# Optimization experiments

Hardware: AMD Instinct MI355X
Metric: run time of the kernel (lower is better)

Reference implementation:

```python
import jax, jax.numpy as jnp
import numpy as np

H = 256   # hidden_size
IN = 2    # adding-problem input features
B, T = 128, 1024


def setup_inputs() -> dict:
    key = jax.random.key(0)
    ks = jax.random.split(key, 12)
    sc = 1.0 / np.sqrt(H)
    u = lambda k, shape: jax.random.uniform(k, shape, minval=-sc, maxval=sc, dtype=jnp.float32)
    return {
        "x": jax.random.normal(ks[0], (B, T, IN), dtype=jnp.float32),
        # GRU weights (torch layout: [3H, in], gate order r, z, n)
        "W_ih": u(ks[1], (3 * H, IN)),
        "W_hh": u(ks[2], (3 * H, H)),
        "b_ih": u(ks[3], (3 * H,)),
        "b_hh": u(ks[4], (3 * H,)),
        # adaptive momentum coefficient beta_t = sigmoid(x W + h U + b)
        "Wb_x": u(ks[5], (IN, 1)),
        "Wb_h": u(ks[6], (H, 1)),
        "b_beta": jnp.zeros((1,), dtype=jnp.float32),
        # momentum step size s (learnable scalar)
        "s": jnp.ones((), dtype=jnp.float32),
        # read-out head Linear(H, 1)
        "W_head": u(ks[7], (1, H)),
        "b_head": u(ks[8], (1,)),
    }


def reference(x, W_ih, W_hh, b_ih, b_hh, Wb_x, Wb_h, b_beta, s, W_head, b_head):
    Bm = x.shape[0]

    def step(carry, x_t):
        h, v = carry                                    # h: [B,H], v: [B,3H]
        beta = jax.nn.sigmoid(x_t @ Wb_x + h @ Wb_h + b_beta)   # [B,1]
        p = x_t @ W_ih.T + b_ih                         # input projection [B,3H]
        v = beta * v + s * p                            # momentum buffer
        gh = h @ W_hh.T + b_hh                          # hidden projection [B,3H]
        vr, vz, vn = jnp.split(v, 3, axis=-1)
        hr, hz, hn = jnp.split(gh, 3, axis=-1)
        r = jax.nn.sigmoid(vr + hr)
        z = jax.nn.sigmoid(vz + hz)
        n = jnp.tanh(vn + r * hn)
        h_new = (1.0 - z) * n + z * h
        return (h_new, v), beta[:, 0]

    h0 = jnp.zeros((Bm, H), dtype=x.dtype)
    v0 = jnp.zeros((Bm, 3 * H), dtype=x.dtype)
    (hT, _), betas = jax.lax.scan(step, (h0, v0), jnp.transpose(x, (1, 0, 2)))
    out = hT @ W_head.T + b_head                        # head on last timestep, [B,1]
    return (out, betas.T)                               # betas: [B,T]
```

## Files before the change

kernel.cpp:

```cpp
#include <hip/hip_runtime.h>

#define HID 256
#define TLEN 1024
#define BATCH 128

typedef _Float16 half2_t __attribute__((ext_vector_type(2)));

__device__ __forceinline__ float fexp2(float x) { return __builtin_amdgcn_exp2f(x); }
__device__ __forceinline__ float frcp(float x)  { return __builtin_amdgcn_rcpf(x); }
__device__ __forceinline__ float fast_sigmoid(float x) {
  return frcp(1.0f + fexp2(-1.442695040888963f * x));
}
__device__ __forceinline__ float fast_tanh(float x) {
  float e = fexp2(2.885390081777927f * x);
  return 1.0f - 2.0f * frcp(e + 1.0f);
}
__device__ __forceinline__ float dot2acc(half2_t a, half2_t b, float c) {
  return __builtin_amdgcn_fdot2(a, b, c, false);
}

#if defined(__has_builtin) && __has_builtin(__builtin_amdgcn_sdot4)
#define SDOT4(a, b, c) __builtin_amdgcn_sdot4((int)(a), (int)(b), (c), false)
#else
__device__ __forceinline__ int SDOT4(int a, int b, int c) {
#pragma unroll
  for (int e = 0; e < 4; ++e)
    c += ((a << (24 - 8 * e)) >> 24) * ((b << (24 - 8 * e)) >> 24);
  return c;
}
#endif

#define DPP_ADD_F(var, ctrl, rmask)                                            \
  var += __builtin_bit_cast(float, __builtin_amdgcn_update_dpp(                \
      0, __builtin_bit_cast(int, var), (ctrl), (rmask), 0xf, true))

__device__ __forceinline__ float wave_sum63_f(float p) {
  DPP_ADD_F(p, 0x111, 0xf);
  DPP_ADD_F(p, 0x112, 0xf);
  DPP_ADD_F(p, 0x114, 0xf);
  DPP_ADD_F(p, 0x118, 0xf);
  DPP_ADD_F(p, 0x142, 0xa);
  DPP_ADD_F(p, 0x143, 0xc);
  return p;
}

__global__ void quant_whh(const float* __restrict__ W_hh,
                          uint4* __restrict__ wq,
                          float* __restrict__ scales) {
  const int r = blockIdx.x * 256 + threadIdx.x;
  const float* row = W_hh + (size_t)r * HID;
  float amax = 0.0f;
  for (int k = 0; k < HID; ++k) amax = fmaxf(amax, fabsf(row[k]));
  amax = fmaxf(amax, 1e-20f);
  scales[r] = amax / 127.0f;
  const float inv = 127.0f / amax;
  for (int c = 0; c < 16; ++c) {
    unsigned w[4];
#pragma unroll
    for (int u = 0; u < 4; ++u) {
      unsigned bb = 0;
#pragma unroll
      for (int e = 0; e < 4; ++e) {
        int qv = (int)rintf(row[16 * c + 4 * u + e] * inv);
        bb |= (unsigned)(qv & 0xff) << (8 * e);
      }
      w[u] = bb;
    }
    wq[(size_t)r * 16 + c] = uint4{w[0], w[1], w[2], w[3]};
  }
}

__global__
__attribute__((amdgpu_flat_work_group_size(768, 768)))
void momgru_persistent(const float* __restrict__ x,
                       const float* __restrict__ W_ih,
                       const float* __restrict__ b_ih,
                       const float* __restrict__ b_hh,
                       const float* __restrict__ Wb_x,
                       const float* __restrict__ Wb_h,
                       const float* __restrict__ b_beta,
                       const float* __restrict__ s_ptr,
                       const float* __restrict__ W_head,
                       const float* __restrict__ b_head,
                       const uint4* __restrict__ wq,
                       const float* __restrict__ scales,
                       float* __restrict__ out)
{
  const int b    = blockIdx.x;
  const int tid  = threadIdx.x;
  const int lane = tid & 63;
  const int wv   = tid >> 6;
  const int g    = tid >> 8;
  const int d    = tid & 255;

  __shared__ __align__(16) unsigned hq[64];
  __shared__ float  rz[2][256];
  __shared__ float4 red4;
  __shared__ float  headred[4];

  const uint4* wqt = wq + (size_t)tid * 16;
  uint4 w[16];
#pragma unroll
  for (int j = 0; j < 16; ++j) w[j] = wqt[j];

  const float sv = s_ptr[0];
  const half2_t wih2 = half2_t{(_Float16)(sv * W_ih[2 * tid]),
                               (_Float16)(sv * W_ih[2 * tid + 1])};
  const float bih = sv * b_ih[tid];
  const float bhh = b_hh[tid];
  const float sc  = scales[tid] * (1.0f / 127.0f);
  const half2_t wbx2 = half2_t{(_Float16)Wb_x[0], (_Float16)Wb_x[1]};
  const float bbeta = b_beta[0];
  const float wbh   = Wb_h[d];

  if (tid < 64) hq[tid] = 0u;
  if (tid == 0) red4 = make_float4(bbeta, 0.0f, 0.0f, 0.0f);
  float v = 0.0f, h_old = 0.0f;
  float* betas = out + BATCH;
  const float2* xg2 = reinterpret_cast<const float2*>(x + (size_t)b * TLEN * 2);
  float2 xv = xg2[0];
  __syncthreads();

  for (int t = 0; t < TLEN; ++t) {
    const float4 rr = red4;
    const float hwb = (rr.x + rr.y) + (rr.z + rr.w);
    const half2_t x2 = half2_t{(_Float16)xv.x, (_Float16)xv.y};
    xv = xg2[(t + 1 < TLEN) ? t + 1 : t];
    const float beta = fast_sigmoid(dot2acc(x2, wbx2, hwb));
    v = beta * v + dot2acc(x2, wih2, bih);
    if (tid == 0) betas[(size_t)b * TLEN + t] = beta;

    const int4* hb = reinterpret_cast<const int4*>(hq);
    int a0 = 0, a1 = 0, a2 = 0, a3 = 0;
#pragma unroll
    for (int c = 0; c < 4; ++c) {
      const int4 h0 = hb[4 * c + 0];
      const int4 h1 = hb[4 * c + 1];
      const int4 h2 = hb[4 * c + 2];
      const int4 h3 = hb[4 * c + 3];
      a0 = SDOT4(h0.x, w[4 * c + 0].x, a0);
      a1 = SDOT4(h1.x, w[4 * c + 1].x, a1);
      a2 = SDOT4(h2.x, w[4 * c + 2].x, a2);
      a3 = SDOT4(h3.x, w[4 * c + 3].x, a3);
      a0 = SDOT4(h0.y, w[4 * c + 0].y, a0);
      a1 = SDOT4(h1.y, w[4 * c + 1].y, a1);
      a2 = SDOT4(h2.y, w[4 * c + 2].y, a2);
      a3 = SDOT4(h3.y, w[4 * c + 3].y, a3);
      a0 = SDOT4(h0.z, w[4 * c + 0].z, a0);
      a1 = SDOT4(h1.z, w[4 * c + 1].z, a1);
      a2 = SDOT4(h2.z, w[4 * c + 2].z, a2);
      a3 = SDOT4(h3.z, w[4 * c + 3].z, a3);
      a0 = SDOT4(h0.w, w[4 * c + 0].w, a0);
      a1 = SDOT4(h1.w, w[4 * c + 1].w, a1);
      a2 = SDOT4(h2.w, w[4 * c + 2].w, a2);
      a3 = SDOT4(h3.w, w[4 * c + 3].w, a3);
    }
    const int a = (a0 + a1) + (a2 + a3);
    const float ga = fmaf((float)a, sc, bhh);

    if (g < 2) rz[g][d] = fast_sigmoid(v + ga);
    __syncthreads();

    if (g == 2) {
      const float r_ = rz[0][d];
      const float z_ = rz[1][d];
      const float n_ = fast_tanh(fmaf(r_, ga, v));
      h_old = fmaf(z_, h_old - n_, n_);
      const int q = (int)rintf(h_old * 127.0f);
      reinterpret_cast<unsigned char*>(hq)[d] = (unsigned char)(q & 0xff);
      float p = h_old * wbh;
      p = wave_sum63_f(p);
      if (lane == 63) {
        const float pv = (wv == 8) ? p + bbeta : p;
        reinterpret_cast<float*>(&red4)[wv - 8] = pv;
      }
    }
    __syncthreads();
  }

  if (g == 2) {
    float hp = h_old * W_head[d];
    hp = wave_sum63_f(hp);
    if (lane == 63) headred[wv - 8] = hp;
  }
  __syncthreads();
  if (tid == 0)
    out[b] = ((headred[0] + headred[1]) + (headred[2] + headred[3])) + b_head[0];
}

extern "C" void kernel_launch(void* const* d_in, const int* in_sizes, int n_in,
                              void* d_out, int out_size, void* d_ws, size_t ws_size,
                              hipStream_t stream) {
  const float* x      = (const float*)d_in[0];
  const float* W_ih   = (const float*)d_in[1];
  const float* W_hh   = (const float*)d_in[2];
  const float* b_ih   = (const float*)d_in[3];
  const float* b_hh   = (const float*)d_in[4];
  const float* Wb_x   = (const float*)d_in[5];
  const float* Wb_h   = (const float*)d_in[6];
  const float* b_beta = (const float*)d_in[7];
  const float* s      = (const float*)d_in[8];
  const float* W_head = (const float*)d_in[9];
  const float* b_head = (const float*)d_in[10];
  float* out = (float*)d_out;

  char* wsb = (char*)d_ws;
  uint4* wq     = (uint4*)wsb;
  float* scales = (float*)(wsb + 196608);

  quant_whh<<<dim3(3), dim3(256), 0, stream>>>(W_hh, wq, scales);
  momgru_persistent<<<dim3(BATCH), dim3(768), 0, stream>>>(
      x, W_ih, b_ih, b_hh, Wb_x, Wb_h, b_beta, s, W_head, b_head,
      (const uint4*)wq, (const float*)scales, out);
}
```

Before: 997.4 us.

## Compute beta reduction redundantly per wave from int8 hidden state, drop shared red4

Quantizes Wb_h to int8 in the prep kernel, and each wave now computes h·Wb_h itself from the shared int8 hidden state with sdot4 and a DPP wave reduction. This replaces the per-step float reduction in the g==2 waves and the shared red4 handoff. The beta and momentum computation moves after the W_hh dot product so it overlaps, and the r/z shared buffer is interleaved so one float2 load serves both gates. It also pins waves_per_eu and uses asm barriers to keep weights in registers. The cost is extra per-wave redundant work and int8 quantization error in beta.

New measurement: 1.026 ms. 2.9% more time.

```diff
diff --git a/kernel.cpp b/kernel.cpp
--- a/kernel.cpp
+++ b/kernel.cpp
@@ -33,6 +33,8 @@
 #define DPP_ADD_F(var, ctrl, rmask)                                            \
   var += __builtin_bit_cast(float, __builtin_amdgcn_update_dpp(                \
       0, __builtin_bit_cast(int, var), (ctrl), (rmask), 0xf, true))
+#define DPP_ADD_I(var, ctrl, rmask)                                            \
+  var += __builtin_amdgcn_update_dpp(0, (var), (ctrl), (rmask), 0xf, true)
 
 __device__ __forceinline__ float wave_sum63_f(float p) {
   DPP_ADD_F(p, 0x111, 0xf);
@@ -43,47 +45,77 @@
   DPP_ADD_F(p, 0x143, 0xc);
   return p;
 }
+__device__ __forceinline__ int wave_sum63_i(int p) {
+  DPP_ADD_I(p, 0x111, 0xf);
+  DPP_ADD_I(p, 0x112, 0xf);
+  DPP_ADD_I(p, 0x114, 0xf);
+  DPP_ADD_I(p, 0x118, 0xf);
+  DPP_ADD_I(p, 0x142, 0xa);
+  DPP_ADD_I(p, 0x143, 0xc);
+  return p;
+}
 
 __global__ void quant_whh(const float* __restrict__ W_hh,
+                          const float* __restrict__ Wb_h,
                           uint4* __restrict__ wq,
-                          float* __restrict__ scales) {
+                          float* __restrict__ scales,
+                          unsigned* __restrict__ wbq,
+                          float* __restrict__ wbscale) {
   const int r = blockIdx.x * 256 + threadIdx.x;
-  const float* row = W_hh + (size_t)r * HID;
-  float amax = 0.0f;
-  for (int k = 0; k < HID; ++k) amax = fmaxf(amax, fabsf(row[k]));
-  amax = fmaxf(amax, 1e-20f);
-  scales[r] = amax / 127.0f;
-  const float inv = 127.0f / amax;
-  for (int c = 0; c < 16; ++c) {
-    unsigned w[4];
-#pragma unroll
-    for (int u = 0; u < 4; ++u) {
-      unsigned bb = 0;
-#pragma unroll
-      for (int e = 0; e < 4; ++e) {
-        int qv = (int)rintf(row[16 * c + 4 * u + e] * inv);
-        bb |= (unsigned)(qv & 0xff) << (8 * e);
+  if (r < 768) {
+    const float* row = W_hh + (size_t)r * HID;
+    float amax = 0.0f;
+    for (int k = 0; k < HID; ++k) amax = fmaxf(amax, fabsf(row[k]));
+    amax = fmaxf(amax, 1e-20f);
+    scales[r] = amax / 127.0f;
+    const float inv = 127.0f / amax;
+    for (int c = 0; c < 16; ++c) {
+      unsigned w[4];
+#pragma unroll
+      for (int u = 0; u < 4; ++u) {
+        unsigned bb = 0;
+#pragma unroll
+        for (int e = 0; e < 4; ++e) {
+          int qv = (int)rintf(row[16 * c + 4 * u + e] * inv);
+          bb |= (unsigned)(qv & 0xff) << (8 * e);
+        }
+        w[u] = bb;
       }
-      w[u] = bb;
-    }
-    wq[(size_t)r * 16 + c] = uint4{w[0], w[1], w[2], w[3]};
+      wq[(size_t)r * 16 + c] = uint4{w[0], w[1], w[2], w[3]};
+    }
+  } else if (r < 832) {
+    float amax = 0.0f;
+    for (int k = 0; k < HID; ++k) amax = fmaxf(amax, fabsf(Wb_h[k]));
+    amax = fmaxf(amax, 1e-20f);
+    const float inv = 127.0f / amax;
+    const int i = r - 768;
+    unsigned bb = 0;
+#pragma unroll
+    for (int e = 0; e < 4; ++e) {
+      int qv = (int)rintf(Wb_h[4 * i + e] * inv);
+      bb |= (unsigned)(qv & 0xff) << (8 * e);
+    }
+    wbq[i] = bb;
+    if (i == 0) wbscale[0] = (amax / 127.0f) * (1.0f / 127.0f);
   }
 }
 
 __global__
 __attribute__((amdgpu_flat_work_group_size(768, 768)))
+__attribute__((amdgpu_waves_per_eu(3, 3)))
 void momgru_persistent(const float* __restrict__ x,
                        const float* __restrict__ W_ih,
                        const float* __restrict__ b_ih,
                        const float* __restrict__ b_hh,
                        const float* __restrict__ Wb_x,
-                       const float* __restrict__ Wb_h,
                        const float* __restrict__ b_beta,
                        const float* __restrict__ s_ptr,
                        const float* __restrict__ W_head,
                        const float* __restrict__ b_head,
                        const uint4* __restrict__ wq,
                        const float* __restrict__ scales,
+                       const unsigned* __restrict__ wbq,
+                       const float* __restrict__ wbscale,
                        float* __restrict__ out)
 {
   const int b    = blockIdx.x;
@@ -94,14 +126,16 @@
   const int d    = tid & 255;
 
   __shared__ __align__(16) unsigned hq[64];
-  __shared__ float  rz[2][256];
-  __shared__ float4 red4;
-  __shared__ float  headred[4];
+  __shared__ float rz2[256][2];
+  __shared__ float headred[4];
 
   const uint4* wqt = wq + (size_t)tid * 16;
   uint4 w[16];
 #pragma unroll
   for (int j = 0; j < 16; ++j) w[j] = wqt[j];
+#pragma unroll
+  for (int j = 0; j < 16; ++j)
+    asm volatile("" : "+v"(w[j].x), "+v"(w[j].y), "+v"(w[j].z), "+v"(w[j].w));
 
   const float sv = s_ptr[0];
   const half2_t wih2 = half2_t{(_Float16)(sv * W_ih[2 * tid]),
@@ -111,10 +145,10 @@
   const float sc  = scales[tid] * (1.0f / 127.0f);
   const half2_t wbx2 = half2_t{(_Float16)Wb_x[0], (_Float16)Wb_x[1]};
   const float bbeta = b_beta[0];
-  const float wbh   = Wb_h[d];
+  const unsigned wbq_l = wbq[lane];
+  const float wbsc = wbscale[0];
 
   if (tid < 64) hq[tid] = 0u;
-  if (tid == 0) red4 = make_float4(bbeta, 0.0f, 0.0f, 0.0f);
   float v = 0.0f, h_old = 0.0f;
   float* betas = out + BATCH;
   const float2* xg2 = reinterpret_cast<const float2*>(x + (size_t)b * TLEN * 2);
@@ -122,13 +156,9 @@
   __syncthreads();
 
   for (int t = 0; t < TLEN; ++t) {
-    const float4 rr = red4;
-    const float hwb = (rr.x + rr.y) + (rr.z + rr.w);
-    const half2_t x2 = half2_t{(_Float16)xv.x, (_Float16)xv.y};
-    xv = xg2[(t + 1 < TLEN) ? t + 1 : t];
-    const float beta = fast_sigmoid(dot2acc(x2, wbx2, hwb));
-    v = beta * v + dot2acc(x2, wih2, bih);
-    if (tid == 0) betas[(size_t)b * TLEN + t] = beta;
+    const unsigned hw_l = reinterpret_cast<const unsigned*>(hq)[lane];
+    int hwb_i = SDOT4(hw_l, wbq_l, 0);
+    hwb_i = wave_sum63_i(hwb_i);
 
     const int4* hb = reinterpret_cast<const int4*>(hq);
     int a0 = 0, a1 = 0, a2 = 0, a3 = 0;
@@ -158,22 +188,22 @@
     const int a = (a0 + a1) + (a2 + a3);
     const float ga = fmaf((float)a, sc, bhh);
 
-    if (g < 2) rz[g][d] = fast_sigmoid(v + ga);
+    const float hWb = (float)__builtin_amdgcn_readlane(hwb_i, 63) * wbsc;
+    const half2_t x2 = half2_t{(_Float16)xv.x, (_Float16)xv.y};
+    xv = xg2[(t + 1 < TLEN) ? t + 1 : t];
+    const float beta = fast_sigmoid(dot2acc(x2, wbx2, hWb + bbeta));
+    v = beta * v + dot2acc(x2, wih2, bih);
+    if (tid == 0) betas[(size_t)b * TLEN + t] = beta;
+
+    if (g < 2) rz2[d][g] = fast_sigmoid(v + ga);
     __syncthreads();
 
     if (g == 2) {
-      const float r_ = rz[0][d];
-      const float z_ = rz[1][d];
-      const float n_ = fast_tanh(fmaf(r_, ga, v));
-      h_old = fmaf(z_, h_old - n_, n_);
+      const float2 rzv = *reinterpret_cast<const float2*>(&rz2[d][0]);
+      const float n_ = fast_tanh(fmaf(rzv.x, ga, v));
+      h_old = fmaf(rzv.y, h_old - n_, n_);
       const int q = (int)rintf(h_old * 127.0f);
       reinterpret_cast<unsigned char*>(hq)[d] = (unsigned char)(q & 0xff);
-      float p = h_old * wbh;
-      p = wave_sum63_f(p);
-      if (lane == 63) {
-        const float pv = (wv == 8) ? p + bbeta : p;
-        reinterpret_cast<float*>(&red4)[wv - 8] = pv;
-      }
     }
     __syncthreads();
   }
@@ -205,11 +235,14 @@
   float* out = (float*)d_out;
 
   char* wsb = (char*)d_ws;
-  uint4* wq     = (uint4*)wsb;
-  float* scales = (float*)(wsb + 196608);
-
-  quant_whh<<<dim3(3), dim3(256), 0, stream>>>(W_hh, wq, scales);
+  uint4*    wq      = (uint4*)wsb;
+  float*    scales  = (float*)(wsb + 196608);
+  unsigned* wbq     = (unsigned*)(wsb + 199680);
+  float*    wbscale = (float*)(wsb + 199936);
+
+  quant_whh<<<dim3(4), dim3(256), 0, stream>>>(W_hh, Wb_h, wq, scales, wbq, wbscale);
   momgru_persistent<<<dim3(BATCH), dim3(768), 0, stream>>>(
-      x, W_ih, b_ih, b_hh, Wb_x, Wb_h, b_beta, s, W_head, b_head,
-      (const uint4*)wq, (const float*)scales, out);
-}
+      x, W_ih, b_ih, b_hh, Wb_x, b_beta, s, W_head, b_head,
+      (const uint4*)wq, (const float*)scales, (const unsigned*)wbq,
+      (const float*)wbscale, out);
+}
```
